# Kernel optimization log

Measured on AMD Instinct MI355X. Metric: run time of the kernel, lower is better.

The kernel has to match this reference:

```python
import jax, jax.numpy as jnp
import numpy as np

NUM_HEADS = 4
K_CLOSEST = 8
LN_EPS = 1e-5

B, N_REC, N_KP, F = 8, 4096, 20, 256


def setup_inputs() -> dict:
    key = jax.random.key(0)
    ks = jax.random.split(key, 5)
    h_rec = jax.random.normal(ks[0], (B, N_REC, F), dtype=jnp.float32)
    x_rec = jax.random.normal(ks[1], (B, N_REC, 3), dtype=jnp.float32) * 3.0
    h0_kp = jax.random.normal(ks[2], (B, N_KP, F), dtype=jnp.float32)
    # fc_src (shared for src and dst, bias=False): in_feats -> out_feats*num_heads
    W_src = jax.random.normal(ks[3], (F, F * NUM_HEADS), dtype=jnp.float32) / np.sqrt(F)
    # kp_feature_mlp: Linear(out_feats + k_closest, out_feats) + SiLU
    W_mlp = jax.random.normal(ks[4], (F + K_CLOSEST, F), dtype=jnp.float32) / np.sqrt(F + K_CLOSEST)
    b_mlp = jnp.zeros((F,), dtype=jnp.float32)
    ln_gamma = jnp.ones((F,), dtype=jnp.float32)
    ln_beta = jnp.zeros((F,), dtype=jnp.float32)
    return {"h_rec": h_rec, "x_rec": x_rec, "h0_kp": h0_kp, "W_src": W_src,
            "W_mlp": W_mlp, "b_mlp": b_mlp, "ln_gamma": ln_gamma, "ln_beta": ln_beta}


def reference(h_rec, x_rec, h0_kp, W_src, W_mlp, b_mlp, ln_gamma, ln_beta):
    Bb, Nr, Fd = h_rec.shape
    Nk = h0_kp.shape[1]
    H = NUM_HEADS
    D = W_src.shape[1] // H  # out_feats per head

    # fc_src applied to both rec and kp features (matches source, fc_dst unused)
    ft_src = (h_rec @ W_src).reshape(Bb, Nr, H, D)   # [B, Nr, H, D]
    ft_dst = (h0_kp @ W_src).reshape(Bb, Nk, H, D)   # [B, Nk, H, D]

    # per-edge dot-product scores over the complete bipartite rec->kp graph
    a = jnp.einsum('brhd,bkhd->brkh', ft_src, ft_dst) / jnp.sqrt(jnp.float32(D))
    a = jnp.exp(a)  # source uses plain exp (no max subtraction)
    sa = a / jnp.sum(a, axis=1, keepdims=True)        # segment softmax over rec atoms per kp

    # attention-weighted aggregation of rec positions, mean over heads
    agg = jnp.einsum('brkh,brc->bkhc', sa, x_rec)     # [B, Nk, H, 3]
    kp_pos = agg.mean(axis=2)                          # [B, Nk, 3]

    # k-closest rec atoms per keypoint
    x_diff = x_rec[:, None, :, :] - kp_pos[:, :, None, :]          # [B, Nk, Nr, 3]
    dist = jnp.sqrt(jnp.sum((x_diff + 1e-30) ** 2, axis=-1))       # [B, Nk, Nr]
    neg_dk, idx = jax.lax.top_k(-dist, K_CLOSEST)                  # idx: [B, Nk, K]
    d_k = -neg_dk                                                  # [B, Nk, K]

    # mean of rec features over the k nearest atoms (per-batch gather)
    h_knn = jax.vmap(lambda h, i: h[i])(h_rec, idx)                # [B, Nk, K, F]
    h_m = h_knn.mean(axis=2)                                       # [B, Nk, F]

    feat_in = jnp.concatenate([h_m, d_k], axis=-1)                 # [B, Nk, F+K]
    kp_feat = jax.nn.silu(feat_in @ W_mlp + b_mlp)

    # LayerNorm (norm=True)
    mu = kp_feat.mean(axis=-1, keepdims=True)
    var = kp_feat.var(axis=-1, keepdims=True)
    kp_feat = (kp_feat - mu) * jax.lax.rsqrt(var + LN_EPS) * ln_gamma + ln_beta
    return kp_pos, kp_feat
```

## Files before the change

### kernel.cpp

```cpp
#include <hip/hip_runtime.h>
#include <math.h>

static constexpr int NB  = 8;
static constexpr int NRC = 4096;
static constexpr int NKP = 20;
static constexpr int NF  = 256;
static constexpr int NHD = 4;
static constexpr int NKH = NKP * NHD;
static constexpr int KCL = 8;
static constexpr int NT  = 16;
static constexpr float SCALE = 0.0625f;

static constexpr int WT_OFF = 0;
static constexpr int M_OFF  = 262144;
static constexpr int P_OFF  = 0;

__global__ __launch_bounds__(256) void k0_transpose(const float* __restrict__ W,
                                                    float* __restrict__ WT) {
    __shared__ float tile[32][65];
    int c0 = (blockIdx.x & 15) * 64;
    int f0 = (blockIdx.x >> 4) * 32;
    int lx = threadIdx.x & 63, ly = threadIdx.x >> 6;
#pragma unroll
    for (int rr = 0; rr < 8; ++rr) {
        int fr = ly + rr * 4;
        tile[fr][lx] = W[(f0 + fr) * 1024 + c0 + lx];
    }
    __syncthreads();
    int lf = threadIdx.x & 31, cy = threadIdx.x >> 5;
#pragma unroll
    for (int rr = 0; rr < 8; ++rr) {
        int cr = cy + rr * 8;
        WT[(c0 + cr) * 256 + f0 + lf] = tile[lf][cr];
    }
}

__global__ __launch_bounds__(512) void k12_m(const float* __restrict__ h0,
                                             const float* __restrict__ W,
                                             const float* __restrict__ WT,
                                             float* __restrict__ M) {
    int bx = blockIdx.x;
    int b = bx / NKP, k = bx % NKP;
    int tid = threadIdx.x;
    __shared__ float h0l[NF];
    __shared__ float ftl[1024];
    if (tid < NF) h0l[tid] = h0[(b * NKP + k) * NF + tid];
    __syncthreads();
    {
        float a0 = 0.f, a1 = 0.f;
        const float* wp = W + tid;
#pragma unroll 4
        for (int g = 0; g < NF; ++g) {
            float hg = h0l[g];
            a0 += hg * wp[g * 1024];
            a1 += hg * wp[g * 1024 + 512];
        }
        ftl[tid] = a0;
        ftl[tid + 512] = a1;
    }
    __syncthreads();
    {
        int f = tid & 255, h = tid >> 8;
        float a0 = 0.f, a1 = 0.f;
        const float* wt0 = WT + (h * 256) * 256 + f;
        const float* wt1 = WT + ((h + 2) * 256) * 256 + f;
        const float* f0p = ftl + h * 256;
        const float* f1p = ftl + (h + 2) * 256;
#pragma unroll 4
        for (int d = 0; d < 256; ++d) {
            a0 += f0p[d] * wt0[d * 256];
            a1 += f1p[d] * wt1[d * 256];
        }
        M[((size_t)b * NKH + k * NHD + h) * NF + f]     = a0 * SCALE;
        M[((size_t)b * NKH + k * NHD + h + 2) * NF + f] = a1 * SCALE;
    }
}

__global__ __launch_bounds__(512) void k3_scores(const float* __restrict__ hrec,
                                                 const float* __restrict__ xrec,
                                                 const float* __restrict__ Mg,
                                                 float* __restrict__ P) {
    __shared__ float Ml[40 * 256];
    int bx = blockIdx.x;
    int b = bx >> 5;
    int rem = bx & 31;
    int t = rem >> 1;
    int g = rem & 1;
    int tid = threadIdx.x;

    const float4* Mg4 = (const float4*)(Mg + ((size_t)b * NKH + g * 40) * NF);
    float4* Ml4 = (float4*)Ml;
#pragma unroll
    for (int i = 0; i < 5; ++i)
        Ml4[i * 512 + tid] = Mg4[i * 512 + tid];
    __syncthreads();

    int w = tid >> 6, lane = tid & 63;
    int c0 = w * 5;
    int r0 = t * 256 + lane * 4;

    float acc[5][4];
#pragma unroll
    for (int c = 0; c < 5; ++c)
#pragma unroll
        for (int r = 0; r < 4; ++r) acc[c][r] = 0.f;

    const float4* A = (const float4*)(hrec + ((size_t)b * NRC + r0) * NF);
    const float* Mlc = Ml + c0 * NF;

#pragma unroll 2
    for (int f4 = 0; f4 < 64; ++f4) {
        float4 a0 = A[f4];
        float4 a1 = A[64 + f4];
        float4 a2 = A[128 + f4];
        float4 a3 = A[192 + f4];
#pragma unroll
        for (int c = 0; c < 5; ++c) {
            float4 m = *(const float4*)(Mlc + c * NF + f4 * 4);
            acc[c][0] += a0.x * m.x + a0.y * m.y + a0.z * m.z + a0.w * m.w;
            acc[c][1] += a1.x * m.x + a1.y * m.y + a1.z * m.z + a1.w * m.w;
            acc[c][2] += a2.x * m.x + a2.y * m.y + a2.z * m.z + a2.w * m.w;
            acc[c][3] += a3.x * m.x + a3.y * m.y + a3.z * m.z + a3.w * m.w;
        }
    }

    const float4* X = (const float4*)(xrec + ((size_t)b * NRC + r0) * 3);
    float4 x0 = X[0], x1 = X[1], x2 = X[2];
    float xs[4] = {x0.x, x0.w, x1.z, x2.y};
    float ys[4] = {x0.y, x1.x, x1.w, x2.z};
    float zs[4] = {x0.z, x1.y, x2.x, x2.w};

    float* Pp = P + ((size_t)(b * NT + t) * NKH + g * 40 + c0) * 4;
#pragma unroll
    for (int c = 0; c < 5; ++c) {
        float e0 = __expf(acc[c][0]), e1 = __expf(acc[c][1]);
        float e2 = __expf(acc[c][2]), e3 = __expf(acc[c][3]);
        float s0 = e0 + e1 + e2 + e3;
        float s1 = e0 * xs[0] + e1 * xs[1] + e2 * xs[2] + e3 * xs[3];
        float s2 = e0 * ys[0] + e1 * ys[1] + e2 * ys[2] + e3 * ys[3];
        float s3 = e0 * zs[0] + e1 * zs[1] + e2 * zs[2] + e3 * zs[3];
#pragma unroll
        for (int m = 1; m < 64; m <<= 1) {
            s0 += __shfl_xor(s0, m, 64);
            s1 += __shfl_xor(s1, m, 64);
            s2 += __shfl_xor(s2, m, 64);
            s3 += __shfl_xor(s3, m, 64);
        }
        if (lane == 0) {
            Pp[c * 4 + 0] = s0; Pp[c * 4 + 1] = s1;
            Pp[c * 4 + 2] = s2; Pp[c * 4 + 3] = s3;
        }
    }
}

#define CSWAP(i, j)                                                         \
    if (d[j] < d[i] || (d[j] == d[i] && ix[j] < ix[i])) {                   \
        float td = d[i]; d[i] = d[j]; d[j] = td;                            \
        int ti = ix[i]; ix[i] = ix[j]; ix[j] = ti;                          \
    }

__global__ __launch_bounds__(512) void k4_final(const float* __restrict__ hrec,
                                                const float* __restrict__ xrec,
                                                const float* __restrict__ P,
                                                const float* __restrict__ Wm,
                                                const float* __restrict__ bm,
                                                const float* __restrict__ gam,
                                                const float* __restrict__ bet,
                                                float* __restrict__ out) {
    int bx = blockIdx.x;
    int b = bx / NKP, k = bx % NKP;
    int tid = threadIdx.x;
    int w = tid >> 6, lane = tid & 63;

    __shared__ float Sh[16];
    __shared__ float posl[4];
    __shared__ float redv[8];
    __shared__ int   redi[8];
    __shared__ int   kidxs[KCL];
    __shared__ float fin[NF + KCL];
    __shared__ float part[2][NF];
    __shared__ float wred[8][2];
    __shared__ float stat[2];

    if (tid < 16) {
        int h = tid >> 2, s = tid & 3;
        float a = 0.f;
#pragma unroll
        for (int t = 0; t < NT; ++t)
            a += P[((b * NT + t) * NKH + k * NHD + h) * 4 + s];
        Sh[tid] = a;
    }
    __syncthreads();
    if (tid == 0) {
#pragma unroll
        for (int c = 0; c < 3; ++c) {
            float p = 0.f;
#pragma unroll
            for (int h = 0; h < NHD; ++h) p += Sh[h * 4 + c + 1] / Sh[h * 4];
            p *= 0.25f;
            posl[c] = p;
            out[(b * NKP + k) * 3 + c] = p;
        }
    }
    __syncthreads();

    float px = posl[0], py = posl[1], pz = posl[2];
    float d[8];
    int ix[8];
#pragma unroll
    for (int s = 0; s < 8; ++s) {
        int i = s * 512 + tid;
        const float* x = xrec + ((size_t)b * NRC + i) * 3;
        float dx = x[0] - px, dy = x[1] - py, dz = x[2] - pz;
        d[s] = dx * dx + dy * dy + dz * dz;
        ix[s] = i;
    }
    CSWAP(0, 1) CSWAP(2, 3) CSWAP(4, 5) CSWAP(6, 7)
    CSWAP(0, 2) CSWAP(1, 3) CSWAP(4, 6) CSWAP(5, 7)
    CSWAP(1, 2) CSWAP(5, 6)
    CSWAP(0, 4) CSWAP(1, 5) CSWAP(2, 6) CSWAP(3, 7)
    CSWAP(2, 4) CSWAP(3, 5)
    CSWAP(1, 2) CSWAP(3, 4) CSWAP(5, 6)

    for (int j = 0; j < KCL; ++j) {
        float bd = d[0];
        int bi = ix[0];
#pragma unroll
        for (int m = 1; m < 64; m <<= 1) {
            float od = __shfl_xor(bd, m, 64);
            int oi = __shfl_xor(bi, m, 64);
            if (od < bd || (od == bd && oi < bi)) { bd = od; bi = oi; }
        }
        if (lane == 0) { redv[w] = bd; redi[w] = bi; }
        __syncthreads();
        bd = redv[0]; bi = redi[0];
#pragma unroll
        for (int q = 1; q < 8; ++q) {
            float od = redv[q]; int oi = redi[q];
            if (od < bd || (od == bd && oi < bi)) { bd = od; bi = oi; }
        }
        if (tid == 0) { kidxs[j] = bi; fin[NF + j] = sqrtf(bd); }
        if (ix[0] == bi) {
#pragma unroll
            for (int s = 0; s < 7; ++s) { d[s] = d[s + 1]; ix[s] = ix[s + 1]; }
            d[7] = 3.4e38f; ix[7] = 0x7fffffff;
        }
        __syncthreads();
    }

    if (tid < NF) {
        float hm = 0.f;
#pragma unroll
        for (int j = 0; j < KCL; ++j)
            hm += hrec[((size_t)b * NRC + kidxs[j]) * NF + tid];
        fin[tid] = hm * 0.125f;
    }
    __syncthreads();

    {
        int o = tid & 255, p = tid >> 8;
        float acc = 0.f;
        const float* wp = Wm + o;
#pragma unroll 2
        for (int i = p * 132; i < p * 132 + 132; ++i)
            acc += fin[i] * wp[i * NF];
        part[p][o] = acc;
    }
    __syncthreads();

    float v = 0.f;
    if (tid < NF) {
        float psum = bm[tid] + part[0][tid] + part[1][tid];
        v = psum / (1.f + __expf(-psum));
    }
    float s = v, sq = v * v;
#pragma unroll
    for (int m = 1; m < 64; m <<= 1) {
        s += __shfl_xor(s, m, 64);
        sq += __shfl_xor(sq, m, 64);
    }
    if (lane == 0) { wred[w][0] = s; wred[w][1] = sq; }
    __syncthreads();
    if (tid == 0) {
        float ts = 0.f, tq = 0.f;
#pragma unroll
        for (int q = 0; q < 8; ++q) { ts += wred[q][0]; tq += wred[q][1]; }
        float mu = ts / 256.f;
        float var = tq / 256.f - mu * mu;
        stat[0] = mu;
        stat[1] = rsqrtf(var + 1e-5f);
    }
    __syncthreads();
    if (tid < NF) {
        float o = (v - stat[0]) * stat[1] * gam[tid] + bet[tid];
        out[NB * NKP * 3 + (b * NKP + k) * NF + tid] = o;
    }
}

extern "C" void kernel_launch(void* const* d_in, const int* in_sizes, int n_in,
                              void* d_out, int out_size, void* d_ws, size_t ws_size,
                              hipStream_t stream) {
    const float* h_rec = (const float*)d_in[0];
    const float* x_rec = (const float*)d_in[1];
    const float* h0_kp = (const float*)d_in[2];
    const float* W_src = (const float*)d_in[3];
    const float* W_mlp = (const float*)d_in[4];
    const float* b_mlp = (const float*)d_in[5];
    const float* gam   = (const float*)d_in[6];
    const float* bet   = (const float*)d_in[7];
    float* outp = (float*)d_out;
    float* ws = (float*)d_ws;

    float* WT = ws + WT_OFF;
    float* M  = ws + M_OFF;
    float* P  = ws + P_OFF;

    hipLaunchKernelGGL(k0_transpose, dim3(128), dim3(256), 0, stream, W_src, WT);
    hipLaunchKernelGGL(k12_m, dim3(160), dim3(512), 0, stream, h0_kp, W_src, WT, M);
    hipLaunchKernelGGL(k3_scores, dim3(256), dim3(512), 0, stream,
                       h_rec, x_rec, M, P);
    hipLaunchKernelGGL(k4_final, dim3(160), dim3(512), 0, stream,
                       h_rec, x_rec, P, W_mlp, b_mlp, gam, bet, outp);
}
```

Baseline: 232.6 us.

## Restructure score kernel to stage h_rec tiles in LDS with atomic reductions

The score kernel now stages 64-row h_rec tiles into swizzled shared memory in two passes, so each block covers all 80 key-head columns. M is read from a transposed global layout instead of being copied into LDS. Partial softmax sums are accumulated with atomicAdd into a zeroed buffer, which removes the per-tile reduction in the final kernel. The M-building kernel is also split across twice as many blocks. This cuts redundant h_rec reads and raises parallelism, at the cost of a memset launch, atomic contention and non-deterministic summation order.

```diff
diff --git a/kernel.cpp b/kernel.cpp
--- a/kernel.cpp
+++ b/kernel.cpp
@@ -8,12 +8,13 @@
 static constexpr int NHD = 4;
 static constexpr int NKH = NKP * NHD;
 static constexpr int KCL = 8;
-static constexpr int NT  = 16;
 static constexpr float SCALE = 0.0625f;
 
 static constexpr int WT_OFF = 0;
-static constexpr int M_OFF  = 262144;
-static constexpr int P_OFF  = 0;
+static constexpr int MT_OFF = 262144;
+static constexpr int MT_CNT = NB * 64 * 8 * 48;
+static constexpr int P_OFF  = MT_OFF + MT_CNT;
+static constexpr int P_CNT  = NB * NKH * 4;
 
 __global__ __launch_bounds__(256) void k0_transpose(const float* __restrict__ W,
                                                     float* __restrict__ WT) {
@@ -38,107 +39,86 @@
 __global__ __launch_bounds__(512) void k12_m(const float* __restrict__ h0,
                                              const float* __restrict__ W,
                                              const float* __restrict__ WT,
-                                             float* __restrict__ M) {
+                                             float* __restrict__ Mt) {
     int bx = blockIdx.x;
-    int b = bx / NKP, k = bx % NKP;
+    int b = bx / 40;
+    int rem = bx % 40;
+    int k = rem >> 1, hp = rem & 1;
     int tid = threadIdx.x;
     __shared__ float h0l[NF];
-    __shared__ float ftl[1024];
+    __shared__ float ftl[512];
     if (tid < NF) h0l[tid] = h0[(b * NKP + k) * NF + tid];
     __syncthreads();
     {
-        float a0 = 0.f, a1 = 0.f;
-        const float* wp = W + tid;
+        float a = 0.f;
+        const float* wp = W + hp * 512 + tid;
 #pragma unroll 4
-        for (int g = 0; g < NF; ++g) {
-            float hg = h0l[g];
-            a0 += hg * wp[g * 1024];
-            a1 += hg * wp[g * 1024 + 512];
-        }
-        ftl[tid] = a0;
-        ftl[tid + 512] = a1;
+        for (int g = 0; g < NF; ++g) a += h0l[g] * wp[g * 1024];
+        ftl[tid] = a;
     }
     __syncthreads();
     {
-        int f = tid & 255, h = tid >> 8;
-        float a0 = 0.f, a1 = 0.f;
-        const float* wt0 = WT + (h * 256) * 256 + f;
-        const float* wt1 = WT + ((h + 2) * 256) * 256 + f;
-        const float* f0p = ftl + h * 256;
-        const float* f1p = ftl + (h + 2) * 256;
+        int f = tid & 255, hh = tid >> 8;
+        int h = hp * 2 + hh;
+        int kh = k * NHD + h;
+        float a = 0.f;
+        const float* wtp = WT + (hp * 512 + hh * 256) * 256 + f;
+        const float* fp = ftl + hh * 256;
 #pragma unroll 4
-        for (int d = 0; d < 256; ++d) {
-            a0 += f0p[d] * wt0[d * 256];
-            a1 += f1p[d] * wt1[d * 256];
-        }
-        M[((size_t)b * NKH + k * NHD + h) * NF + f]     = a0 * SCALE;
-        M[((size_t)b * NKH + k * NHD + h + 2) * NF + f] = a1 * SCALE;
+        for (int d = 0; d < 256; ++d) a += fp[d] * wtp[d * 256];
+        int cg = kh / 10, cw = kh % 10;
+        Mt[(size_t)b * 24576 + (f >> 2) * 384 + cg * 48 + cw * 4 + (f & 3)] = a * SCALE;
     }
 }
 
 __global__ __launch_bounds__(512) void k3_scores(const float* __restrict__ hrec,
                                                  const float* __restrict__ xrec,
-                                                 const float* __restrict__ Mg,
+                                                 const float* __restrict__ Mt,
                                                  float* __restrict__ P) {
-    __shared__ float Ml[40 * 256];
+    __shared__ float4 ldsA[2048];
     int bx = blockIdx.x;
-    int b = bx >> 5;
-    int rem = bx & 31;
-    int t = rem >> 1;
-    int g = rem & 1;
+    int b = bx >> 6, t = bx & 63;
     int tid = threadIdx.x;
-
-    const float4* Mg4 = (const float4*)(Mg + ((size_t)b * NKH + g * 40) * NF);
-    float4* Ml4 = (float4*)Ml;
-#pragma unroll
-    for (int i = 0; i < 5; ++i)
-        Ml4[i * 512 + tid] = Mg4[i * 512 + tid];
-    __syncthreads();
-
-    int w = tid >> 6, lane = tid & 63;
-    int c0 = w * 5;
-    int r0 = t * 256 + lane * 4;
-
-    float acc[5][4];
-#pragma unroll
-    for (int c = 0; c < 5; ++c)
-#pragma unroll
-        for (int r = 0; r < 4; ++r) acc[c][r] = 0.f;
-
-    const float4* A = (const float4*)(hrec + ((size_t)b * NRC + r0) * NF);
-    const float* Mlc = Ml + c0 * NF;
-
+    int r = tid & 63, cg = tid >> 6;
+    int rowbase = t * 64;
+
+    float acc[10];
+#pragma unroll
+    for (int c = 0; c < 10; ++c) acc[c] = 0.f;
+
+    const float* Mb = Mt + (size_t)b * 24576 + cg * 48;
+
+    for (int pass = 0; pass < 2; ++pass) {
+        if (pass) __syncthreads();
+#pragma unroll
+        for (int j = 0; j < 4; ++j) {
+            int c = j * 512 + tid;
+            int row = c >> 5, fc = c & 31;
+            const float4* src = (const float4*)(hrec +
+                ((size_t)(b * NRC + rowbase + row)) * NF + pass * 128 + fc * 4);
+            ldsA[fc * 64 + (row ^ (fc & 7))] = *src;
+        }
+        __syncthreads();
 #pragma unroll 2
-    for (int f4 = 0; f4 < 64; ++f4) {
-        float4 a0 = A[f4];
-        float4 a1 = A[64 + f4];
-        float4 a2 = A[128 + f4];
-        float4 a3 = A[192 + f4];
-#pragma unroll
-        for (int c = 0; c < 5; ++c) {
-            float4 m = *(const float4*)(Mlc + c * NF + f4 * 4);
-            acc[c][0] += a0.x * m.x + a0.y * m.y + a0.z * m.z + a0.w * m.w;
-            acc[c][1] += a1.x * m.x + a1.y * m.y + a1.z * m.z + a1.w * m.w;
-            acc[c][2] += a2.x * m.x + a2.y * m.y + a2.z * m.z + a2.w * m.w;
-            acc[c][3] += a3.x * m.x + a3.y * m.y + a3.z * m.z + a3.w * m.w;
-        }
-    }
-
-    const float4* X = (const float4*)(xrec + ((size_t)b * NRC + r0) * 3);
-    float4 x0 = X[0], x1 = X[1], x2 = X[2];
-    float xs[4] = {x0.x, x0.w, x1.z, x2.y};
-    float ys[4] = {x0.y, x1.x, x1.w, x2.z};
-    float zs[4] = {x0.z, x1.y, x2.x, x2.w};
-
-    float* Pp = P + ((size_t)(b * NT + t) * NKH + g * 40 + c0) * 4;
-#pragma unroll
-    for (int c = 0; c < 5; ++c) {
-        float e0 = __expf(acc[c][0]), e1 = __expf(acc[c][1]);
-        float e2 = __expf(acc[c][2]), e3 = __expf(acc[c][3]);
-        float s0 = e0 + e1 + e2 + e3;
-        float s1 = e0 * xs[0] + e1 * xs[1] + e2 * xs[2] + e3 * xs[3];
-        float s2 = e0 * ys[0] + e1 * ys[1] + e2 * ys[2] + e3 * ys[3];
-        float s3 = e0 * zs[0] + e1 * zs[1] + e2 * zs[2] + e3 * zs[3];
+        for (int fc = 0; fc < 32; ++fc) {
+            float4 a = ldsA[fc * 64 + (r ^ (fc & 7))];
+            const float* mp = Mb + (pass * 32 + fc) * 384;
+#pragma unroll
+            for (int c = 0; c < 10; ++c) {
+                float4 m = *(const float4*)(mp + c * 4);
+                acc[c] += a.x * m.x + a.y * m.y + a.z * m.z + a.w * m.w;
+            }
+        }
+    }
+
+    const float* xr = xrec + ((size_t)(b * NRC + rowbase + r)) * 3;
+    float xx = xr[0], xy = xr[1], xz = xr[2];
+
+    float* Pb = P + (b * NKH + cg * 10) * 4;
+#pragma unroll
+    for (int c = 0; c < 10; ++c) {
+        float e = __expf(acc[c]);
+        float s0 = e, s1 = e * xx, s2 = e * xy, s3 = e * xz;
 #pragma unroll
         for (int m = 1; m < 64; m <<= 1) {
             s0 += __shfl_xor(s0, m, 64);
@@ -146,9 +126,11 @@
             s2 += __shfl_xor(s2, m, 64);
             s3 += __shfl_xor(s3, m, 64);
         }
-        if (lane == 0) {
-            Pp[c * 4 + 0] = s0; Pp[c * 4 + 1] = s1;
-            Pp[c * 4 + 2] = s2; Pp[c * 4 + 3] = s3;
+        if (r == 0) {
+            atomicAdd(&Pb[c * 4 + 0], s0);
+            atomicAdd(&Pb[c * 4 + 1], s1);
+            atomicAdd(&Pb[c * 4 + 2], s2);
+            atomicAdd(&Pb[c * 4 + 3], s3);
         }
     }
 }
@@ -182,14 +164,8 @@
     __shared__ float wred[8][2];
     __shared__ float stat[2];
 
-    if (tid < 16) {
-        int h = tid >> 2, s = tid & 3;
-        float a = 0.f;
-#pragma unroll
-        for (int t = 0; t < NT; ++t)
-            a += P[((b * NT + t) * NKH + k * NHD + h) * 4 + s];
-        Sh[tid] = a;
-    }
+    if (tid < 16)
+        Sh[tid] = P[(b * NKH + k * NHD + (tid >> 2)) * 4 + (tid & 3)];
     __syncthreads();
     if (tid == 0) {
 #pragma unroll
@@ -312,13 +288,14 @@
     float* ws = (float*)d_ws;
 
     float* WT = ws + WT_OFF;
-    float* M  = ws + M_OFF;
+    float* Mt = ws + MT_OFF;
     float* P  = ws + P_OFF;
 
+    hipMemsetAsync(P, 0, P_CNT * sizeof(float), stream);
     hipLaunchKernelGGL(k0_transpose, dim3(128), dim3(256), 0, stream, W_src, WT);
-    hipLaunchKernelGGL(k12_m, dim3(160), dim3(512), 0, stream, h0_kp, W_src, WT, M);
-    hipLaunchKernelGGL(k3_scores, dim3(256), dim3(512), 0, stream,
-                       h_rec, x_rec, M, P);
+    hipLaunchKernelGGL(k12_m, dim3(320), dim3(512), 0, stream, h0_kp, W_src, WT, Mt);
+    hipLaunchKernelGGL(k3_scores, dim3(512), dim3(512), 0, stream,
+                       h_rec, x_rec, Mt, P);
     hipLaunchKernelGGL(k4_final, dim3(160), dim3(512), 0, stream,
                        h_rec, x_rec, P, W_mlp, b_mlp, gam, bet, outp);
 }
```

After: 303.6 us. 30.5% more time.
